# Performance work log

Measured on AMD Instinct MI355X. Metric: run time of the kernel, lower is better.

Reference implementation:

```python
import jax, jax.numpy as jnp
import numpy as np

B, L, DIM, H = 1, 2048, 3072, 24
D = DIM // H  # 128
EPS = 1e-6

def setup_inputs() -> dict:
    key = jax.random.key(0)
    ks = jax.random.split(key, 7)
    x = jax.random.normal(ks[0], (B, L, DIM), dtype=jnp.float32)
    pe = jax.random.normal(ks[1], (B, 1, L, D // 2, 2, 2), dtype=jnp.float32)
    w_qkv = jax.random.normal(ks[2], (DIM, 3 * DIM), dtype=jnp.float32) / np.sqrt(DIM)
    q_scale = jnp.ones((D,), dtype=jnp.float32)
    k_scale = jnp.ones((D,), dtype=jnp.float32)
    w_proj = jax.random.normal(ks[3], (DIM, DIM), dtype=jnp.float32) / np.sqrt(DIM)
    b_proj = jnp.zeros((DIM,), dtype=jnp.float32)
    return {"x": x, "pe": pe, "w_qkv": w_qkv, "q_scale": q_scale,
            "k_scale": k_scale, "w_proj": w_proj, "b_proj": b_proj}

def _rmsnorm(t, scale):
    # flax nn.RMSNorm: t * rsqrt(mean(t^2, -1) + eps) * scale
    ms = jnp.mean(jnp.square(t), axis=-1, keepdims=True)
    return t * jax.lax.rsqrt(ms + EPS) * scale

def _apply_rope(xq, xk, pe):
    # xq/xk: [B,H,L,D]; pe: [B,1,L,D/2,2,2]
    xq_ = xq.reshape(*xq.shape[:-1], -1, 1, 2)
    xk_ = xk.reshape(*xk.shape[:-1], -1, 1, 2)
    xq_out = pe[..., 0] * xq_[..., 0] + pe[..., 1] * xq_[..., 1]
    xk_out = pe[..., 0] * xk_[..., 0] + pe[..., 1] * xk_[..., 1]
    return xq_out.reshape(xq.shape), xk_out.reshape(xk.shape)

def reference(x, pe, w_qkv, q_scale, k_scale, w_proj, b_proj):
    qkv = jnp.einsum('bld,de->ble', x, w_qkv)            # [B,L,3*DIM]
    qkv = qkv.reshape(B, L, 3, H, D)
    qkv = jnp.moveaxis(qkv, 2, 0)                          # [3,B,H?,..]
    q, k, v = jnp.transpose(qkv, (0, 1, 3, 2, 4))          # each [B,H,L,D]
    q = _rmsnorm(q, q_scale).astype(v.dtype)
    k = _rmsnorm(k, k_scale).astype(v.dtype)
    q, k = _apply_rope(q, k, pe)
    scale = 1.0 / np.sqrt(D)
    scores = jnp.einsum('bhqd,bhkd->bhqk', q, k) * scale   # [B,H,L,L]
    attn = jax.nn.softmax(scores, axis=-1)
    out = jnp.einsum('bhqk,bhkd->bhqd', attn, v)           # [B,H,L,D]
    out = jnp.transpose(out, (0, 2, 1, 3)).reshape(B, L, DIM)
    return jnp.einsum('bld,de->ble', out, w_proj) + b_proj
```

## Files before the change

kernel.cpp:

```cpp
#include <hip/hip_runtime.h>

#define L_    2048
#define DIM_  3072
#define H_    24
#define D_    128
#define NQKV  9216

typedef __attribute__((ext_vector_type(8))) short bf16x8;
typedef __attribute__((ext_vector_type(4))) float f32x4;

__device__ __forceinline__ unsigned short f2bf(float f) {
  union { float f; unsigned u; } v; v.f = f;
  unsigned r = v.u + 0x7fffu + ((v.u >> 16) & 1u);
  return (unsigned short)(r >> 16);
}
__device__ __forceinline__ float bf2f(unsigned short h) {
  union { unsigned u; float f; } v; v.u = ((unsigned)h) << 16;
  return v.f;
}

__device__ __forceinline__ void gload_lds16(const void* g, void* l) {
  auto* lp = reinterpret_cast<__attribute__((address_space(3))) unsigned int*>(
      reinterpret_cast<uintptr_t>(l));
  auto* gp = reinterpret_cast<const __attribute__((address_space(1))) unsigned int*>(
      reinterpret_cast<uintptr_t>(g));
  __builtin_amdgcn_global_load_lds(gp, lp, 16, 0, 0);
}

__global__ void cast_f32_to_bf16(const float* __restrict__ in,
                                 unsigned short* __restrict__ out, int n) {
  int total = n >> 2;
  int stride = gridDim.x * blockDim.x;
  for (int i = blockIdx.x * blockDim.x + threadIdx.x; i < total; i += stride) {
    float4 v = ((const float4*)in)[i];
    ushort4 o;
    o.x = f2bf(v.x); o.y = f2bf(v.y); o.z = f2bf(v.z); o.w = f2bf(v.w);
    ((ushort4*)out)[i] = o;
  }
}

__global__ __launch_bounds__(256)
void castT_f32_bf16(const float* __restrict__ in, unsigned short* __restrict__ out,
                    int K, int N) {
  int k = blockIdx.x * 256 + threadIdx.x;
  int n0 = blockIdx.y * 128;
  const float* src = in + (size_t)k * N;
  #pragma unroll 8
  for (int j = 0; j < 128; j++)
    out[(size_t)(n0 + j) * K + k] = f2bf(src[n0 + j]);
}

template<bool OUT_BF16, bool BIAS>
__global__ __launch_bounds__(256, 2)
void gemm_bt(const unsigned short* __restrict__ A,
             const unsigned short* __restrict__ Bt,
             void* __restrict__ Cout, const float* __restrict__ bias,
             int M, int N, int K)
{
  __shared__ unsigned short As[128 * 64];
  __shared__ unsigned short Bs[128 * 64];
  const int tid  = threadIdx.x;
  const int wave = tid >> 6;
  const int lane = tid & 63;
  const int l15  = lane & 15;
  const int quad = lane >> 4;
  const int wm = wave >> 1, wn = wave & 1;
  const int bm = blockIdx.y * 128;
  const int bn = blockIdx.x * 128;

  const int srow = lane >> 3;
  const int scol = (lane & 7) ^ srow;
  const unsigned short* Ag = A  + (size_t)(bm + wave * 32 + srow) * K + scol * 8;
  const unsigned short* Bg = Bt + (size_t)(bn + wave * 32 + srow) * K + scol * 8;
  unsigned short* Al = &As[(wave * 32) * 64];
  unsigned short* Bl = &Bs[(wave * 32) * 64];

  f32x4 acc[4][4];
  #pragma unroll
  for (int i = 0; i < 4; i++)
    #pragma unroll
    for (int j = 0; j < 4; j++) acc[i][j] = (f32x4){0.f, 0.f, 0.f, 0.f};

  for (int k0 = 0; k0 < K; k0 += 64) {
    __syncthreads();
    #pragma unroll
    for (int j = 0; j < 4; j++) {
      gload_lds16(Ag + (size_t)j * 8 * K + k0, Al + j * 8 * 64);
      gload_lds16(Bg + (size_t)j * 8 * K + k0, Bl + j * 8 * 64);
    }
    __syncthreads();
    #pragma unroll
    for (int ks = 0; ks < 2; ks++) {
      const int cph = ((ks * 4 + quad) ^ (l15 & 7)) * 8;
      bf16x8 af[4], bf[4];
      #pragma unroll
      for (int mt = 0; mt < 4; mt++)
        af[mt] = *(const bf16x8*)&As[(wm * 64 + mt * 16 + l15) * 64 + cph];
      #pragma unroll
      for (int nt = 0; nt < 4; nt++)
        bf[nt] = *(const bf16x8*)&Bs[(wn * 64 + nt * 16 + l15) * 64 + cph];
      #pragma unroll
      for (int mt = 0; mt < 4; mt++)
        #pragma unroll
        for (int nt = 0; nt < 4; nt++)
          acc[mt][nt] = __builtin_amdgcn_mfma_f32_16x16x32_bf16(
              af[mt], bf[nt], acc[mt][nt], 0, 0, 0);
    }
  }
  #pragma unroll
  for (int mt = 0; mt < 4; mt++)
    #pragma unroll
    for (int nt = 0; nt < 4; nt++)
      #pragma unroll
      for (int r = 0; r < 4; r++) {
        int row = bm + wm * 64 + mt * 16 + quad * 4 + r;
        int col = bn + wn * 64 + nt * 16 + l15;
        float v = acc[mt][nt][r];
        if (BIAS) v += bias[col];
        if (OUT_BF16)
          ((unsigned short*)Cout)[(size_t)row * N + col] = f2bf(v);
        else
          ((float*)Cout)[(size_t)row * N + col] = v;
      }
}

__global__ __launch_bounds__(128)
void qkv_post(const unsigned short* __restrict__ qkv,
              const float* __restrict__ pe,
              const float* __restrict__ q_scale,
              const float* __restrict__ k_scale,
              unsigned short* __restrict__ Qo,
              unsigned short* __restrict__ Ko)
{
  const int l = blockIdx.x;
  const int h = blockIdx.y;
  const int d = threadIdx.x;
  const int wave = d >> 6;
  const unsigned short* row = qkv + (size_t)l * NQKV + h * D_;
  float qv = bf2f(row[d]);
  float kv = bf2f(row[DIM_ + d]);
  float q2 = qv * qv, k2 = kv * kv;
  #pragma unroll
  for (int mask = 1; mask < 64; mask <<= 1) {
    q2 += __shfl_xor(q2, mask);
    k2 += __shfl_xor(k2, mask);
  }
  __shared__ float sq[2], sk[2];
  __shared__ float qbuf[128], kbuf[128];
  if ((d & 63) == 0) { sq[wave] = q2; sk[wave] = k2; }
  __syncthreads();
  float msq = (sq[0] + sq[1]) * (1.f / 128.f);
  float msk = (sk[0] + sk[1]) * (1.f / 128.f);
  qbuf[d] = qv * rsqrtf(msq + 1e-6f) * q_scale[d];
  kbuf[d] = kv * rsqrtf(msk + 1e-6f) * k_scale[d];
  __syncthreads();
  int p = d >> 1, s = d & 1;
  const float* pel = pe + (((size_t)l * 64 + p) * 2 + s) * 2;
  float a = pel[0], b = pel[1];
  float qr = (a * qbuf[2 * p] + b * qbuf[2 * p + 1]) * 0.08838834764831845f;
  float kr =  a * kbuf[2 * p] + b * kbuf[2 * p + 1];
  size_t o = ((size_t)h * L_ + l) * D_ + d;
  Qo[o] = f2bf(qr);
  Ko[o] = f2bf(kr);
}

__global__ __launch_bounds__(256)
void v_transpose(const unsigned short* __restrict__ qkv,
                 unsigned short* __restrict__ Vt) {
  int h = blockIdx.y;
  int l = blockIdx.x * 256 + threadIdx.x;
  const unsigned short* src = qkv + (size_t)l * NQKV + 2 * DIM_ + h * D_;
  unsigned short* dst = Vt + (size_t)h * D_ * L_ + l;
  #pragma unroll
  for (int c = 0; c < 16; c++) {
    uint4 v = *(const uint4*)&src[c * 8];
    const unsigned short* pv = (const unsigned short*)&v;
    #pragma unroll
    for (int j = 0; j < 8; j++)
      dst[(size_t)(c * 8 + j) * L_] = pv[j];
  }
}

__global__ __launch_bounds__(128, 2)
void flash_attn(const unsigned short* __restrict__ Q,
                const unsigned short* __restrict__ K,
                const unsigned short* __restrict__ Vt,
                unsigned short* __restrict__ Out)
{
  __shared__ unsigned short Ks[64 * 128];
  __shared__ unsigned short Vs[128 * 64];
  __shared__ unsigned short Ps[2][32 * 72];
  const int tid  = threadIdx.x;
  const int wave = tid >> 6;
  const int lane = tid & 63;
  const int l15  = lane & 15;
  const int quad = lane >> 4;
  const int h  = blockIdx.y;
  const int qw = blockIdx.x * 64 + wave * 32;

  const unsigned short* Qh = Q  + (size_t)h * L_ * D_;
  const unsigned short* Kh = K  + (size_t)h * L_ * D_;
  const unsigned short* Vh = Vt + (size_t)h * D_ * L_;

  bf16x8 qf[2][4];
  #pragma unroll
  for (int mt = 0; mt < 2; mt++)
    #pragma unroll
    for (int kc = 0; kc < 4; kc++)
      qf[mt][kc] = *(const bf16x8*)&Qh[(size_t)(qw + mt * 16 + l15) * D_ + kc * 32 + quad * 8];

  const int k_row = lane >> 4;
  const int k_cph = lane & 15;
  const int v_row = lane >> 3;
  const int v_cl  = (lane & 7) ^ v_row;

  f32x4 oacc[2][8];
  #pragma unroll
  for (int i = 0; i < 2; i++)
    #pragma unroll
    for (int j = 0; j < 8; j++) oacc[i][j] = (f32x4){0.f, 0.f, 0.f, 0.f};
  float m_i[2][4], l_i[2][4];
  #pragma unroll
  for (int i = 0; i < 2; i++)
    #pragma unroll
    for (int r = 0; r < 4; r++) { m_i[i][r] = -1e30f; l_i[i][r] = 0.f; }

  for (int t = 0; t < L_; t += 64) {
    __syncthreads();
    #pragma unroll
    for (int j = 0; j < 8; j++) {
      int R  = wave * 32 + j * 4;
      int rl = (R & 15) | k_row;
      int cl = k_cph ^ rl;
      gload_lds16(&Kh[(size_t)(t + R + k_row) * D_ + cl * 8], &Ks[R * 128]);
      int R2 = wave * 64 + j * 8;
      gload_lds16(&Vh[(size_t)(R2 + v_row) * L_ + t + v_cl * 8], &Vs[R2 * 64]);
    }
    __syncthreads();

    f32x4 s[2][4];
    #pragma unroll
    for (int i = 0; i < 2; i++)
      #pragma unroll
      for (int j = 0; j < 4; j++) s[i][j] = (f32x4){0.f, 0.f, 0.f, 0.f};
    #pragma unroll
    for (int nt = 0; nt < 4; nt++) {
      const int krow = nt * 16 + l15;
      #pragma unroll
      for (int kc = 0; kc < 4; kc++) {
        bf16x8 kf = *(const bf16x8*)&Ks[krow * 128 + (((kc * 4 + quad) ^ l15) * 8)];
        s[0][nt] = __builtin_amdgcn_mfma_f32_16x16x32_bf16(qf[0][kc], kf, s[0][nt], 0, 0, 0);
        s[1][nt] = __builtin_amdgcn_mfma_f32_16x16x32_bf16(qf[1][kc], kf, s[1][nt], 0, 0, 0);
      }
    }
    #pragma unroll
    for (int mt = 0; mt < 2; mt++) {
      float rmax[4], alpha[4], rsum[4];
      #pragma unroll
      for (int r = 0; r < 4; r++)
        rmax[r] = fmaxf(fmaxf(s[mt][0][r], s[mt][1][r]), fmaxf(s[mt][2][r], s[mt][3][r]));
      #pragma unroll
      for (int m = 1; m < 16; m <<= 1)
        #pragma unroll
        for (int r = 0; r < 4; r++)
          rmax[r] = fmaxf(rmax[r], __shfl_xor(rmax[r], m));
      #pragma unroll
      for (int r = 0; r < 4; r++) {
        float mnew = fmaxf(m_i[mt][r], rmax[r]);
        alpha[r] = __expf(m_i[mt][r] - mnew);
        m_i[mt][r] = mnew;
        rsum[r] = 0.f;
      }
      #pragma unroll
      for (int nt = 0; nt < 4; nt++)
        #pragma unroll
        for (int r = 0; r < 4; r++) {
          float p = __expf(s[mt][nt][r] - m_i[mt][r]);
          rsum[r] += p;
          Ps[wave][(mt * 16 + quad * 4 + r) * 72 + nt * 16 + l15] = f2bf(p);
        }
      #pragma unroll
      for (int m = 1; m < 16; m <<= 1)
        #pragma unroll
        for (int r = 0; r < 4; r++)
          rsum[r] += __shfl_xor(rsum[r], m);
      #pragma unroll
      for (int r = 0; r < 4; r++)
        l_i[mt][r] = l_i[mt][r] * alpha[r] + rsum[r];
      #pragma unroll
      for (int nt = 0; nt < 8; nt++)
        #pragma unroll
        for (int r = 0; r < 4; r++)
          oacc[mt][nt][r] *= alpha[r];
    }
    asm volatile("s_waitcnt lgkmcnt(0)" ::: "memory");
    bf16x8 pf[2][2];
    #pragma unroll
    for (int mt = 0; mt < 2; mt++)
      #pragma unroll
      for (int ks = 0; ks < 2; ks++)
        pf[mt][ks] = *(const bf16x8*)&Ps[wave][(mt * 16 + l15) * 72 + (ks * 4 + quad) * 8];
    #pragma unroll
    for (int nt = 0; nt < 8; nt++) {
      const int vrow = nt * 16 + l15;
      #pragma unroll
      for (int ks = 0; ks < 2; ks++) {
        bf16x8 vf = *(const bf16x8*)&Vs[vrow * 64 + (((ks * 4 + quad) ^ (l15 & 7)) * 8)];
        oacc[0][nt] = __builtin_amdgcn_mfma_f32_16x16x32_bf16(pf[0][ks], vf, oacc[0][nt], 0, 0, 0);
        oacc[1][nt] = __builtin_amdgcn_mfma_f32_16x16x32_bf16(pf[1][ks], vf, oacc[1][nt], 0, 0, 0);
      }
    }
  }
  #pragma unroll
  for (int mt = 0; mt < 2; mt++)
    #pragma unroll
    for (int nt = 0; nt < 8; nt++)
      #pragma unroll
      for (int r = 0; r < 4; r++) {
        int row = qw + mt * 16 + quad * 4 + r;
        int col = h * D_ + nt * 16 + l15;
        Out[(size_t)row * DIM_ + col] = f2bf(oacc[mt][nt][r] / l_i[mt][r]);
      }
}

extern "C" void kernel_launch(void* const* d_in, const int* in_sizes, int n_in,
                              void* d_out, int out_size, void* d_ws, size_t ws_size,
                              hipStream_t stream) {
  const float* x       = (const float*)d_in[0];
  const float* pe      = (const float*)d_in[1];
  const float* w_qkv   = (const float*)d_in[2];
  const float* q_scale = (const float*)d_in[3];
  const float* k_scale = (const float*)d_in[4];
  const float* w_proj  = (const float*)d_in[5];
  const float* b_proj  = (const float*)d_in[6];

  unsigned short* w_qkvT  = (unsigned short*)d_ws;
  unsigned short* w_projT = w_qkvT + 28311552;
  unsigned short* x_b     = w_projT + 9437184;
  unsigned short* qkv_b   = x_b + 6291456;
  unsigned short* q_r     = qkv_b + 18874368;
  unsigned short* k_r     = q_r + 6291456;
  unsigned short* vt_r    = k_r + 6291456;
  unsigned short* attn_b  = qkv_b;

  cast_f32_to_bf16<<<2048, 256, 0, stream>>>(x, x_b, 6291456);
  castT_f32_bf16<<<dim3(12, 72), 256, 0, stream>>>(w_qkv, w_qkvT, 3072, 9216);
  castT_f32_bf16<<<dim3(12, 24), 256, 0, stream>>>(w_proj, w_projT, 3072, 3072);

  gemm_bt<true, false><<<dim3(72, 16), 256, 0, stream>>>(
      x_b, w_qkvT, qkv_b, nullptr, 2048, 9216, 3072);

  qkv_post<<<dim3(2048, 24), 128, 0, stream>>>(
      qkv_b, pe, q_scale, k_scale, q_r, k_r);
  v_transpose<<<dim3(8, 24), 256, 0, stream>>>(qkv_b, vt_r);

  flash_attn<<<dim3(32, 24), 128, 0, stream>>>(q_r, k_r, vt_r, attn_b);

  gemm_bt<false, true><<<dim3(24, 16), 256, 0, stream>>>(
      attn_b, w_projT, d_out, b_proj, 2048, 3072, 3072);
}
```

Before: 616.4 us.

## Split attention KV tiles across wave pairs and keep P in registers via transposed MFMA

The flash attention kernel now runs four waves per block. Each pair of waves shares a 32-row query group and takes half of every 64-key tile. S is computed transposed (K as the A operand), so the softmax probabilities can feed the PV MFMA straight from registers using the 16x16x16 bf16 instruction, with no LDS round trip for P. At the end, the two partial softmax states are merged through shared memory. The gemm launch bounds also change to ask for 3 blocks per CU. This trades extra merge work and syncs for more parallelism and less LDS traffic, with some risk of register pressure.

```diff
diff --git a/kernel.cpp b/kernel.cpp
--- a/kernel.cpp
+++ b/kernel.cpp
@@ -7,6 +7,7 @@
 #define NQKV  9216
 
 typedef __attribute__((ext_vector_type(8))) short bf16x8;
+typedef __attribute__((ext_vector_type(4))) short bf16x4;
 typedef __attribute__((ext_vector_type(4))) float f32x4;
 
 __device__ __forceinline__ unsigned short f2bf(float f) {
@@ -51,7 +52,7 @@
 }
 
 template<bool OUT_BF16, bool BIAS>
-__global__ __launch_bounds__(256, 2)
+__global__ __launch_bounds__(256, 3)
 void gemm_bt(const unsigned short* __restrict__ A,
              const unsigned short* __restrict__ Bt,
              void* __restrict__ Cout, const float* __restrict__ bias,
@@ -181,22 +182,28 @@
   }
 }
 
-__global__ __launch_bounds__(128, 2)
+__global__ __launch_bounds__(256, 3)
 void flash_attn(const unsigned short* __restrict__ Q,
                 const unsigned short* __restrict__ K,
                 const unsigned short* __restrict__ Vt,
                 unsigned short* __restrict__ Out)
 {
-  __shared__ unsigned short Ks[64 * 128];
-  __shared__ unsigned short Vs[128 * 64];
-  __shared__ unsigned short Ps[2][32 * 72];
+  __shared__ __align__(16) char smem[34304];
+  unsigned short* Ks = (unsigned short*)smem;
+  unsigned short* Vs = Ks + 8192;
+  float*  Obuf = (float*)smem;
+  float2* mlb  = (float2*)(smem + 32768);
+  float4* sAr  = (float4*)(smem + 33280);
+
   const int tid  = threadIdx.x;
   const int wave = tid >> 6;
   const int lane = tid & 63;
   const int l15  = lane & 15;
   const int quad = lane >> 4;
+  const int qg = wave >> 1;
+  const int kh = wave & 1;
   const int h  = blockIdx.y;
-  const int qw = blockIdx.x * 64 + wave * 32;
+  const int q0 = blockIdx.x * 64 + qg * 32;
 
   const unsigned short* Qh = Q  + (size_t)h * L_ * D_;
   const unsigned short* Kh = K  + (size_t)h * L_ * D_;
@@ -204,123 +211,151 @@
 
   bf16x8 qf[2][4];
   #pragma unroll
-  for (int mt = 0; mt < 2; mt++)
+  for (int nt = 0; nt < 2; nt++)
     #pragma unroll
     for (int kc = 0; kc < 4; kc++)
-      qf[mt][kc] = *(const bf16x8*)&Qh[(size_t)(qw + mt * 16 + l15) * D_ + kc * 32 + quad * 8];
-
-  const int k_row = lane >> 4;
-  const int k_cph = lane & 15;
-  const int v_row = lane >> 3;
-  const int v_cl  = (lane & 7) ^ v_row;
+      qf[nt][kc] = *(const bf16x8*)&Qh[(size_t)(q0 + nt * 16 + l15) * D_ + kc * 32 + quad * 8];
 
   f32x4 oacc[2][8];
   #pragma unroll
   for (int i = 0; i < 2; i++)
     #pragma unroll
     for (int j = 0; j < 8; j++) oacc[i][j] = (f32x4){0.f, 0.f, 0.f, 0.f};
-  float m_i[2][4], l_i[2][4];
-  #pragma unroll
-  for (int i = 0; i < 2; i++)
-    #pragma unroll
-    for (int r = 0; r < 4; r++) { m_i[i][r] = -1e30f; l_i[i][r] = 0.f; }
+  float m_i[2] = {-1e30f, -1e30f}, l_i[2] = {0.f, 0.f};
+
+  const int kr_l = lane >> 4;
+  const int vr_l = lane >> 3;
+  const int vcl  = (lane & 7) ^ vr_l;
 
   for (int t = 0; t < L_; t += 64) {
     __syncthreads();
     #pragma unroll
-    for (int j = 0; j < 8; j++) {
-      int R  = wave * 32 + j * 4;
-      int rl = (R & 15) | k_row;
-      int cl = k_cph ^ rl;
-      gload_lds16(&Kh[(size_t)(t + R + k_row) * D_ + cl * 8], &Ks[R * 128]);
-      int R2 = wave * 64 + j * 8;
-      gload_lds16(&Vh[(size_t)(R2 + v_row) * L_ + t + v_cl * 8], &Vs[R2 * 64]);
+    for (int ji = 0; ji < 4; ji++) {
+      int Rr = wave * 16 + ji * 4;
+      int cl = (lane & 15) ^ ((Rr + kr_l) & 15);
+      gload_lds16(&Kh[(size_t)(t + Rr + kr_l) * D_ + cl * 8], &Ks[Rr * 128]);
+      int R2 = wave * 32 + ji * 8;
+      gload_lds16(&Vh[(size_t)(R2 + vr_l) * L_ + t + vcl * 8], &Vs[R2 * 64]);
     }
     __syncthreads();
 
-    f32x4 s[2][4];
+    f32x4 s[2][2];
     #pragma unroll
     for (int i = 0; i < 2; i++)
       #pragma unroll
-      for (int j = 0; j < 4; j++) s[i][j] = (f32x4){0.f, 0.f, 0.f, 0.f};
-    #pragma unroll
-    for (int nt = 0; nt < 4; nt++) {
-      const int krow = nt * 16 + l15;
+      for (int j = 0; j < 2; j++) s[i][j] = (f32x4){0.f, 0.f, 0.f, 0.f};
+    #pragma unroll
+    for (int mt = 0; mt < 2; mt++) {
+      const int krow = kh * 32 + mt * 16 + l15;
       #pragma unroll
       for (int kc = 0; kc < 4; kc++) {
         bf16x8 kf = *(const bf16x8*)&Ks[krow * 128 + (((kc * 4 + quad) ^ l15) * 8)];
-        s[0][nt] = __builtin_amdgcn_mfma_f32_16x16x32_bf16(qf[0][kc], kf, s[0][nt], 0, 0, 0);
-        s[1][nt] = __builtin_amdgcn_mfma_f32_16x16x32_bf16(qf[1][kc], kf, s[1][nt], 0, 0, 0);
+        s[mt][0] = __builtin_amdgcn_mfma_f32_16x16x32_bf16(kf, qf[0][kc], s[mt][0], 0, 0, 0);
+        s[mt][1] = __builtin_amdgcn_mfma_f32_16x16x32_bf16(kf, qf[1][kc], s[mt][1], 0, 0, 0);
       }
     }
-    #pragma unroll
-    for (int mt = 0; mt < 2; mt++) {
-      float rmax[4], alpha[4], rsum[4];
+    float vmax[2], alpha[2], rs[2];
+    #pragma unroll
+    for (int nt = 0; nt < 2; nt++) {
+      vmax[nt] = fmaxf(fmaxf(fmaxf(s[0][nt][0], s[0][nt][1]), fmaxf(s[0][nt][2], s[0][nt][3])),
+                       fmaxf(fmaxf(s[1][nt][0], s[1][nt][1]), fmaxf(s[1][nt][2], s[1][nt][3])));
+      vmax[nt] = fmaxf(vmax[nt], __shfl_xor(vmax[nt], 16));
+      vmax[nt] = fmaxf(vmax[nt], __shfl_xor(vmax[nt], 32));
+      float mnew = fmaxf(m_i[nt], vmax[nt]);
+      alpha[nt] = __expf(m_i[nt] - mnew);
+      m_i[nt] = mnew;
+      rs[nt] = 0.f;
+    }
+    #pragma unroll
+    for (int mt = 0; mt < 2; mt++)
+      #pragma unroll
+      for (int nt = 0; nt < 2; nt++)
+        #pragma unroll
+        for (int r = 0; r < 4; r++) {
+          float p = __expf(s[mt][nt][r] - m_i[nt]);
+          s[mt][nt][r] = p;
+          rs[nt] += p;
+        }
+    #pragma unroll
+    for (int nt = 0; nt < 2; nt++) {
+      rs[nt] += __shfl_xor(rs[nt], 16);
+      rs[nt] += __shfl_xor(rs[nt], 32);
+      l_i[nt] = l_i[nt] * alpha[nt] + rs[nt];
+    }
+    float ar[2][4];
+    #pragma unroll
+    for (int qt = 0; qt < 2; qt++)
       #pragma unroll
       for (int r = 0; r < 4; r++)
-        rmax[r] = fmaxf(fmaxf(s[mt][0][r], s[mt][1][r]), fmaxf(s[mt][2][r], s[mt][3][r]));
-      #pragma unroll
-      for (int m = 1; m < 16; m <<= 1)
+        ar[qt][r] = __shfl(alpha[qt], quad * 4 + r);
+    #pragma unroll
+    for (int qt = 0; qt < 2; qt++)
+      #pragma unroll
+      for (int ntd = 0; ntd < 8; ntd++)
         #pragma unroll
         for (int r = 0; r < 4; r++)
-          rmax[r] = fmaxf(rmax[r], __shfl_xor(rmax[r], m));
+          oacc[qt][ntd][r] *= ar[qt][r];
+    bf16x4 pk[2][2];
+    #pragma unroll
+    for (int mt = 0; mt < 2; mt++)
+      #pragma unroll
+      for (int qt = 0; qt < 2; qt++)
+        pk[mt][qt] = (bf16x4){(short)f2bf(s[mt][qt][0]), (short)f2bf(s[mt][qt][1]),
+                              (short)f2bf(s[mt][qt][2]), (short)f2bf(s[mt][qt][3])};
+    #pragma unroll
+    for (int ntd = 0; ntd < 8; ntd++) {
+      const int vrow = ntd * 16 + l15;
+      #pragma unroll
+      for (int mt = 0; mt < 2; mt++) {
+        int phys = (kh * 4 + mt * 2 + (quad >> 1)) ^ (l15 & 7);
+        bf16x4 vf = *(const bf16x4*)&Vs[vrow * 64 + phys * 8 + (quad & 1) * 4];
+        oacc[0][ntd] = __builtin_amdgcn_mfma_f32_16x16x16bf16_1k(pk[mt][0], vf, oacc[0][ntd], 0, 0, 0);
+        oacc[1][ntd] = __builtin_amdgcn_mfma_f32_16x16x16bf16_1k(pk[mt][1], vf, oacc[1][ntd], 0, 0, 0);
+      }
+    }
+  }
+
+  __syncthreads();
+  if (kh == 1) {
+    #pragma unroll
+    for (int qt = 0; qt < 2; qt++)
+      #pragma unroll
+      for (int ntd = 0; ntd < 8; ntd++)
+        #pragma unroll
+        for (int r = 0; r < 4; r++)
+          Obuf[(size_t)(qg * 32 + qt * 16 + quad * 4 + r) * 128 + ntd * 16 + l15] = oacc[qt][ntd][r];
+    if (quad == 0)
+      #pragma unroll
+      for (int qt = 0; qt < 2; qt++)
+        mlb[qg * 32 + qt * 16 + l15] = make_float2(m_i[qt], l_i[qt]);
+  }
+  __syncthreads();
+  if (kh == 0 && quad == 0) {
+    #pragma unroll
+    for (int qt = 0; qt < 2; qt++) {
+      float2 m1 = mlb[qg * 32 + qt * 16 + l15];
+      float M  = fmaxf(m_i[qt], m1.x);
+      float a0 = __expf(m_i[qt] - M);
+      float a1 = __expf(m1.x - M);
+      float Ls = l_i[qt] * a0 + m1.y * a1;
+      sAr[qg * 32 + qt * 16 + l15] = make_float4(a0, a1, 1.f / Ls, 0.f);
+    }
+  }
+  __syncthreads();
+  if (kh == 0) {
+    #pragma unroll
+    for (int qt = 0; qt < 2; qt++)
       #pragma unroll
       for (int r = 0; r < 4; r++) {
-        float mnew = fmaxf(m_i[mt][r], rmax[r]);
-        alpha[r] = __expf(m_i[mt][r] - mnew);
-        m_i[mt][r] = mnew;
-        rsum[r] = 0.f;
+        float4 A = sAr[qg * 32 + qt * 16 + quad * 4 + r];
+        #pragma unroll
+        for (int ntd = 0; ntd < 8; ntd++) {
+          float o1 = Obuf[(size_t)(qg * 32 + qt * 16 + quad * 4 + r) * 128 + ntd * 16 + l15];
+          float v  = (oacc[qt][ntd][r] * A.x + o1 * A.y) * A.z;
+          Out[(size_t)(q0 + qt * 16 + quad * 4 + r) * DIM_ + h * D_ + ntd * 16 + l15] = f2bf(v);
+        }
       }
-      #pragma unroll
-      for (int nt = 0; nt < 4; nt++)
-        #pragma unroll
-        for (int r = 0; r < 4; r++) {
-          float p = __expf(s[mt][nt][r] - m_i[mt][r]);
-          rsum[r] += p;
-          Ps[wave][(mt * 16 + quad * 4 + r) * 72 + nt * 16 + l15] = f2bf(p);
-        }
-      #pragma unroll
-      for (int m = 1; m < 16; m <<= 1)
-        #pragma unroll
-        for (int r = 0; r < 4; r++)
-          rsum[r] += __shfl_xor(rsum[r], m);
-      #pragma unroll
-      for (int r = 0; r < 4; r++)
-        l_i[mt][r] = l_i[mt][r] * alpha[r] + rsum[r];
-      #pragma unroll
-      for (int nt = 0; nt < 8; nt++)
-        #pragma unroll
-        for (int r = 0; r < 4; r++)
-          oacc[mt][nt][r] *= alpha[r];
-    }
-    asm volatile("s_waitcnt lgkmcnt(0)" ::: "memory");
-    bf16x8 pf[2][2];
-    #pragma unroll
-    for (int mt = 0; mt < 2; mt++)
-      #pragma unroll
-      for (int ks = 0; ks < 2; ks++)
-        pf[mt][ks] = *(const bf16x8*)&Ps[wave][(mt * 16 + l15) * 72 + (ks * 4 + quad) * 8];
-    #pragma unroll
-    for (int nt = 0; nt < 8; nt++) {
-      const int vrow = nt * 16 + l15;
-      #pragma unroll
-      for (int ks = 0; ks < 2; ks++) {
-        bf16x8 vf = *(const bf16x8*)&Vs[vrow * 64 + (((ks * 4 + quad) ^ (l15 & 7)) * 8)];
-        oacc[0][nt] = __builtin_amdgcn_mfma_f32_16x16x32_bf16(pf[0][ks], vf, oacc[0][nt], 0, 0, 0);
-        oacc[1][nt] = __builtin_amdgcn_mfma_f32_16x16x32_bf16(pf[1][ks], vf, oacc[1][nt], 0, 0, 0);
-      }
-    }
-  }
-  #pragma unroll
-  for (int mt = 0; mt < 2; mt++)
-    #pragma unroll
-    for (int nt = 0; nt < 8; nt++)
-      #pragma unroll
-      for (int r = 0; r < 4; r++) {
-        int row = qw + mt * 16 + quad * 4 + r;
-        int col = h * D_ + nt * 16 + l15;
-        Out[(size_t)row * DIM_ + col] = f2bf(oacc[mt][nt][r] / l_i[mt][r]);
-      }
+  }
 }
 
 extern "C" void kernel_launch(void* const* d_in, const int* in_sizes, int n_in,
@@ -354,7 +389,7 @@
       qkv_b, pe, q_scale, k_scale, q_r, k_r);
   v_transpose<<<dim3(8, 24), 256, 0, stream>>>(qkv_b, vt_r);
 
-  flash_attn<<<dim3(32, 24), 128, 0, stream>>>(q_r, k_r, vt_r, attn_b);
+  flash_attn<<<dim3(32, 24), 256, 0, stream>>>(q_r, k_r, vt_r, attn_b);
 
   gemm_bt<false, true><<<dim3(24, 16), 256, 0, stream>>>(
       attn_b, w_projT, d_out, b_proj, 2048, 3072, 3072);
```

New measurement: 559.5 us. 1.1x faster.
